# Optimization experiments

Hardware: AMD Instinct MI355X
Metric: run time of the kernel (lower is better)

Reference implementation:

```python
import jax, jax.numpy as jnp
import numpy as np

WINDOW = 128  # crop size (compute_crops default window_size)


def centre_crop(centroids, window_size, h, w):
    # centroids: [C,2] int; returns flat gather coords [2, C*ws*ws]
    half = window_size // 2
    cy = jnp.clip(centroids[:, 0], half, h - half)
    cx = jnp.clip(centroids[:, 1], half, w - half)
    gy, gx = jnp.meshgrid(jnp.arange(window_size), jnp.arange(window_size), indexing='ij')
    rows = (cy - half)[:, None, None] + gy[None]  # [C,ws,ws]
    cols = (cx - half)[:, None, None] + gx[None]
    return jnp.stack([rows.reshape(-1), cols.reshape(-1)])  # [2, C*ws*ws]


def setup_inputs() -> dict:
    key = jax.random.key(0)
    ks = jax.random.split(key, 8)
    E, S, C, H, W = 6, 1, 512, 1024, 1024
    Dh = 16
    return {
        'x': jax.random.normal(ks[0], (E, H, W), dtype=jnp.float32),
        'sigma': jax.random.uniform(ks[1], (S, H, W), dtype=jnp.float32),
        'c': jax.random.normal(ks[2], (C, E), dtype=jnp.float32),
        'W1': jax.random.normal(ks[3], (E + S, Dh), dtype=jnp.float32) * 0.3,
        'b1': jnp.zeros((Dh,), dtype=jnp.float32),
        'W2': jax.random.normal(ks[4], (Dh, Dh), dtype=jnp.float32) * 0.3,
        'b2': jnp.zeros((Dh,), dtype=jnp.float32),
        'W3': jax.random.normal(ks[5], (Dh, 1), dtype=jnp.float32) * 0.3,
        'b3': jnp.zeros((1,), dtype=jnp.float32),
        'centroids_idx': jax.random.randint(ks[6], (C, 2), 0, H, dtype=jnp.int32),
    }


def reference(x, sigma, c, W1, b1, W2, b2, W3, b3, centroids_idx):
    E, h, w = x.shape
    S = sigma.shape[0]
    C = c.shape[0]
    ws = WINDOW
    mesh = centre_crop(centroids_idx, ws, h, w)  # [2, C*ws*ws]
    # gather per-instance windows from concatenated embedding+sigma maps
    xs = jnp.concatenate([x, sigma], axis=0)  # [E+S, H, W]
    g = xs[:, mesh[0], mesh[1]]               # [E+S, C*ws*ws]
    g = g.reshape(E + S, C, ws, ws).transpose(1, 0, 2, 3)  # [C, E+S, ws, ws]
    # subtract centroid descriptor from embedding channels (feature_engineering '0')
    g = jnp.concatenate([g[:, :E] - c[:, :, None, None], g[:, E:]], axis=1)
    feats = g.transpose(0, 2, 3, 1).reshape(-1, E + S)  # [(C*ws*ws), E+S]
    # per-pixel probability MLP (ProbabilityNet)
    hdn = jax.nn.relu(feats @ W1 + b1)
    hdn = jax.nn.relu(hdn @ W2 + b2)
    prob = jax.nn.sigmoid(hdn @ W3 + b3)
    prob = prob.reshape(C, 1, ws, ws)
    # instance-id / coordinate table for the downstream scatter (iidd)
    inst = jnp.repeat(jnp.arange(C, dtype=mesh.dtype), ws * ws)
    iidd = jnp.concatenate([inst[None], mesh], axis=0)  # [3, C*ws*ws]
    return prob, iidd
```

## Files before the change

kernel.cpp:

```cpp
#include <hip/hip_runtime.h>

#define HW (1024 * 1024)
#define PLANE 8388608

typedef _Float16 half4 __attribute__((ext_vector_type(4)));
typedef _Float16 half8 __attribute__((ext_vector_type(8)));
typedef float floatx4 __attribute__((ext_vector_type(4)));

__global__ __launch_bounds__(256) void prep(
    const float* __restrict__ x,
    const float* __restrict__ sigma,
    const float* __restrict__ W1,
    const int*   __restrict__ cent,
    _Float16* __restrict__ P,
    float* __restrict__ out)
{
    if (blockIdx.x < 4096) {
        const int px = blockIdx.x * 256 + threadIdx.x;
        float g[7];
#pragma unroll
        for (int e = 0; e < 6; ++e) g[e] = x[e * HW + px];
        g[6] = sigma[px];

        half8 lo, hi;
#pragma unroll
        for (int j = 0; j < 16; ++j) {
            float a = 0.0f;
#pragma unroll
            for (int e = 0; e < 7; ++e)
                a = fmaf(g[e], W1[e * 16 + j], a);
            if (j < 8) lo[j] = (_Float16)a; else hi[j - 8] = (_Float16)a;
        }
        *(half8*)(P + (size_t)px * 16)     = lo;
        *(half8*)(P + (size_t)px * 16 + 8) = hi;
    } else {
        const int b   = blockIdx.x - 4096;
        const int w   = b >> 2;
        const int qtr = b & 3;
        const int cy0 = min(max(cent[2 * w], 64), 960) - 64;
        const int cx0 = min(max(cent[2 * w + 1], 64), 960) - 64;
        const float iw = (float)w;
#pragma unroll
        for (int pass = 0; pass < 4; ++pass) {
            const int p = qtr * 4096 + pass * 1024 + threadIdx.x * 4;
            const int n = w * 16384 + p;
            const float row = (float)(cy0 + (p >> 7));
            const float c0  = (float)(cx0 + (p & 127));
            float4 iv = {iw, iw, iw, iw};
            float4 rv = {row, row, row, row};
            float4 cv = {c0, c0 + 1.0f, c0 + 2.0f, c0 + 3.0f};
            *(float4*)(out + PLANE + n)     = iv;
            *(float4*)(out + 2 * PLANE + n) = rv;
            *(float4*)(out + 3 * PLANE + n) = cv;
        }
    }
}

__global__ __launch_bounds__(256) void instanseg_mlp(
    const _Float16* __restrict__ P,
    const float* __restrict__ c,
    const float* __restrict__ W1,
    const float* __restrict__ b1,
    const float* __restrict__ W2,
    const float* __restrict__ b2,
    const float* __restrict__ W3,
    const float* __restrict__ b3,
    const int*   __restrict__ cent,
    float* __restrict__ out)
{
    const int cid  = blockIdx.y;
    const int lane = threadIdx.x & 63;
    const int wave = threadIdx.x >> 6;
    const int quad = lane >> 4;
    const int sub  = lane & 15;

    const int cy0 = min(max(cent[2 * cid], 64), 960) - 64;
    const int cx0 = min(max(cent[2 * cid + 1], 64), 960) - 64;

    half4 a2, qh;
    float w3f[4], bb2[4];
#pragma unroll
    for (int i = 0; i < 4; ++i) {
        const int k = 4 * quad + i;
        a2[i]  = (_Float16)W2[k * 16 + sub];
        w3f[i] = W3[k];
        bb2[i] = b2[k];
        float qv = -b1[k];
#pragma unroll
        for (int e = 0; e < 6; ++e)
            qv = fmaf(W1[e * 16 + k], c[cid * 6 + e], qv);
        qh[i] = (_Float16)qv;
    }
    const float b3v = b3[0];
    const floatx4 zero = {0.0f, 0.0f, 0.0f, 0.0f};
    const int wavestart = blockIdx.x * 2048 + wave * 512;

#pragma unroll 2
    for (int it = 0; it < 8; ++it) {
        const int start = wavestart + it * 64;
        const int srcbase = (cy0 + (start >> 7)) * 1024 + cx0 + (start & 127);
        const _Float16* pb = P + (size_t)(srcbase + sub) * 16 + quad * 4;

        float logit[4];
#pragma unroll
        for (int ch = 0; ch < 4; ++ch) {
            half4 v = *(const half4*)(pb + ch * 256);
            half4 h = v - qh;
#pragma unroll
            for (int i = 0; i < 4; ++i)
                h[i] = h[i] > (_Float16)0.0f ? h[i] : (_Float16)0.0f;

            floatx4 c2 = __builtin_amdgcn_mfma_f32_16x16x16f16(a2, h, zero, 0, 0, 0);

            float part = 0.0f;
#pragma unroll
            for (int i = 0; i < 4; ++i)
                part = fmaf(w3f[i], fmaxf(c2[i] + bb2[i], 0.0f), part);
            part += __shfl_xor(part, 16, 64);
            part += __shfl_xor(part, 32, 64);
            logit[ch] = part;
        }

        const float l01 = (quad & 1) ? logit[1] : logit[0];
        const float l23 = (quad & 1) ? logit[3] : logit[2];
        const float lg  = (quad & 2) ? l23 : l01;
        const float prob = __builtin_amdgcn_rcpf(1.0f + __expf(-(lg + b3v)));

        out[cid * 16384 + start + lane] = prob;
    }
}

extern "C" void kernel_launch(void* const* d_in, const int* in_sizes, int n_in,
                              void* d_out, int out_size, void* d_ws, size_t ws_size,
                              hipStream_t stream) {
    const float* x     = (const float*)d_in[0];
    const float* sigma = (const float*)d_in[1];
    const float* c     = (const float*)d_in[2];
    const float* W1    = (const float*)d_in[3];
    const float* b1    = (const float*)d_in[4];
    const float* W2    = (const float*)d_in[5];
    const float* b2    = (const float*)d_in[6];
    const float* W3    = (const float*)d_in[7];
    const float* b3    = (const float*)d_in[8];
    const int*   cent  = (const int*)d_in[9];
    float* out = (float*)d_out;
    _Float16* P = (_Float16*)d_ws;

    prep<<<dim3(4096 + 2048), dim3(256), 0, stream>>>(x, sigma, W1, cent, P, out);
    instanseg_mlp<<<dim3(8, 512), dim3(256), 0, stream>>>(
        P, c, W1, b1, W2, b2, W3, b3, cent, out);
}
```

Measured before the change: 209.2 us.

## Fuse first-layer projection into per-crop MLP kernel using LDS tiles

Replaces the two-kernel scheme (precompute a full-image fp16 first-layer projection into a workspace, then run the MLP per crop) with one fused kernel. Each block loads a 16-row strip of a crop from x and sigma, computes the first layer into shared memory, then runs the MFMA-based second and third layers from LDS. The index-table writes move into an extra z-slice of the same grid. This removes the 32 MB workspace write and read, but the first layer is now recomputed for every overlapping crop (512 crops of 128x128 pixels each), and the grid's x dimension of 8 column blocks mostly exits early.

Measured after the change: 258.4 us. +23.5%, slower.

```diff
diff --git a/kernel.cpp b/kernel.cpp
--- a/kernel.cpp
+++ b/kernel.cpp
@@ -7,57 +7,9 @@
 typedef _Float16 half8 __attribute__((ext_vector_type(8)));
 typedef float floatx4 __attribute__((ext_vector_type(4)));
 
-__global__ __launch_bounds__(256) void prep(
+__global__ __launch_bounds__(512) void instanseg_fused(
     const float* __restrict__ x,
     const float* __restrict__ sigma,
-    const float* __restrict__ W1,
-    const int*   __restrict__ cent,
-    _Float16* __restrict__ P,
-    float* __restrict__ out)
-{
-    if (blockIdx.x < 4096) {
-        const int px = blockIdx.x * 256 + threadIdx.x;
-        float g[7];
-#pragma unroll
-        for (int e = 0; e < 6; ++e) g[e] = x[e * HW + px];
-        g[6] = sigma[px];
-
-        half8 lo, hi;
-#pragma unroll
-        for (int j = 0; j < 16; ++j) {
-            float a = 0.0f;
-#pragma unroll
-            for (int e = 0; e < 7; ++e)
-                a = fmaf(g[e], W1[e * 16 + j], a);
-            if (j < 8) lo[j] = (_Float16)a; else hi[j - 8] = (_Float16)a;
-        }
-        *(half8*)(P + (size_t)px * 16)     = lo;
-        *(half8*)(P + (size_t)px * 16 + 8) = hi;
-    } else {
-        const int b   = blockIdx.x - 4096;
-        const int w   = b >> 2;
-        const int qtr = b & 3;
-        const int cy0 = min(max(cent[2 * w], 64), 960) - 64;
-        const int cx0 = min(max(cent[2 * w + 1], 64), 960) - 64;
-        const float iw = (float)w;
-#pragma unroll
-        for (int pass = 0; pass < 4; ++pass) {
-            const int p = qtr * 4096 + pass * 1024 + threadIdx.x * 4;
-            const int n = w * 16384 + p;
-            const float row = (float)(cy0 + (p >> 7));
-            const float c0  = (float)(cx0 + (p & 127));
-            float4 iv = {iw, iw, iw, iw};
-            float4 rv = {row, row, row, row};
-            float4 cv = {c0, c0 + 1.0f, c0 + 2.0f, c0 + 3.0f};
-            *(float4*)(out + PLANE + n)     = iv;
-            *(float4*)(out + 2 * PLANE + n) = rv;
-            *(float4*)(out + 3 * PLANE + n) = cv;
-        }
-    }
-}
-
-__global__ __launch_bounds__(256) void instanseg_mlp(
-    const _Float16* __restrict__ P,
     const float* __restrict__ c,
     const float* __restrict__ W1,
     const float* __restrict__ b1,
@@ -68,14 +20,67 @@
     const int*   __restrict__ cent,
     float* __restrict__ out)
 {
-    const int cid  = blockIdx.y;
+    __shared__ _Float16 PL[16 * 128 * 16];
+
+    if (blockIdx.z == 8) {
+        const int id  = blockIdx.x + 8 * blockIdx.y;
+        const int w   = id >> 3;
+        const int oct = id & 7;
+        const int cy0 = min(max(cent[2 * w], 64), 960) - 64;
+        const int cx0 = min(max(cent[2 * w + 1], 64), 960) - 64;
+        const int p   = oct * 2048 + threadIdx.x * 4;
+        const int n   = w * 16384 + p;
+        const float iw  = (float)w;
+        const float row = (float)(cy0 + (p >> 7));
+        const float c0  = (float)(cx0 + (p & 127));
+        float4 iv = {iw, iw, iw, iw};
+        float4 rv = {row, row, row, row};
+        float4 cv = {c0, c0 + 1.0f, c0 + 2.0f, c0 + 3.0f};
+        *(float4*)(out + PLANE + n)     = iv;
+        *(float4*)(out + 2 * PLANE + n) = rv;
+        *(float4*)(out + 3 * PLANE + n) = cv;
+        return;
+    }
+
+    const int d = blockIdx.x;
+    const int w = blockIdx.y;
+    const int g = blockIdx.z;
+
+    const int cy0 = min(max(cent[2 * w], 64), 960) - 64;
+    const int cx0 = min(max(cent[2 * w + 1], 64), 960) - 64;
+
+    const int gr0 = cy0 + 16 * g;
+    const int r0  = max(gr0, 128 * d);
+    const int r1  = min(gr0 + 16, 128 * d + 128);
+    if (r0 >= r1) return;
+    const int nrows = r1 - r0;
+    const int npx   = nrows * 128;
+
+    for (int p = threadIdx.x; p < npx; p += 512) {
+        const int src = (r0 + (p >> 7)) * 1024 + cx0 + (p & 127);
+        float gch[7];
+#pragma unroll
+        for (int e = 0; e < 6; ++e) gch[e] = x[e * HW + src];
+        gch[6] = sigma[src];
+
+        half8 lo, hi;
+#pragma unroll
+        for (int j = 0; j < 16; ++j) {
+            float a = 0.0f;
+#pragma unroll
+            for (int e = 0; e < 7; ++e)
+                a = fmaf(gch[e], W1[e * 16 + j], a);
+            if (j < 8) lo[j] = (_Float16)a; else hi[j - 8] = (_Float16)a;
+        }
+        *(half8*)(PL + p * 16)     = lo;
+        *(half8*)(PL + p * 16 + 8) = hi;
+    }
+    __syncthreads();
+
     const int lane = threadIdx.x & 63;
     const int wave = threadIdx.x >> 6;
     const int quad = lane >> 4;
     const int sub  = lane & 15;
-
-    const int cy0 = min(max(cent[2 * cid], 64), 960) - 64;
-    const int cx0 = min(max(cent[2 * cid + 1], 64), 960) - 64;
 
     half4 a2, qh;
     float w3f[4], bb2[4];
@@ -88,23 +93,21 @@
         float qv = -b1[k];
 #pragma unroll
         for (int e = 0; e < 6; ++e)
-            qv = fmaf(W1[e * 16 + k], c[cid * 6 + e], qv);
+            qv = fmaf(W1[e * 16 + k], c[w * 6 + e], qv);
         qh[i] = (_Float16)qv;
     }
     const float b3v = b3[0];
     const floatx4 zero = {0.0f, 0.0f, 0.0f, 0.0f};
-    const int wavestart = blockIdx.x * 2048 + wave * 512;
 
-#pragma unroll 2
-    for (int it = 0; it < 8; ++it) {
-        const int start = wavestart + it * 64;
-        const int srcbase = (cy0 + (start >> 7)) * 1024 + cx0 + (start & 127);
-        const _Float16* pb = P + (size_t)(srcbase + sub) * 16 + quad * 4;
+    const int wrbase = r0 - cy0;
+    const int n_iter = nrows * 2;
 
+    for (int it = wave; it < n_iter; it += 8) {
+        const int p0 = it * 64;
         float logit[4];
 #pragma unroll
         for (int ch = 0; ch < 4; ++ch) {
-            half4 v = *(const half4*)(pb + ch * 256);
+            half4 v = *(const half4*)(PL + (p0 + ch * 16 + sub) * 16 + quad * 4);
             half4 h = v - qh;
 #pragma unroll
             for (int i = 0; i < 4; ++i)
@@ -126,7 +129,8 @@
         const float lg  = (quad & 2) ? l23 : l01;
         const float prob = __builtin_amdgcn_rcpf(1.0f + __expf(-(lg + b3v)));
 
-        out[cid * 16384 + start + lane] = prob;
+        const int pl = p0 + lane;
+        out[w * 16384 + (wrbase + (pl >> 7)) * 128 + (pl & 127)] = prob;
     }
 }
 
@@ -144,9 +148,7 @@
     const float* b3    = (const float*)d_in[8];
     const int*   cent  = (const int*)d_in[9];
     float* out = (float*)d_out;
-    _Float16* P = (_Float16*)d_ws;
 
-    prep<<<dim3(4096 + 2048), dim3(256), 0, stream>>>(x, sigma, W1, cent, P, out);
-    instanseg_mlp<<<dim3(8, 512), dim3(256), 0, stream>>>(
-        P, c, W1, b1, W2, b2, W3, b3, cent, out);
+    instanseg_fused<<<dim3(8, 512, 9), dim3(512), 0, stream>>>(
+        x, sigma, c, W1, b1, W2, b2, W3, b3, cent, out);
 }
```

## Bin MLP tiles by source row band for locality and move iidd writes into MLP kernel

Applied to the files above, without the earlier changes.

A new single-block kernel buckets each (instance, 16-row group) tile into one of 8 bands by its source row position. The MLP grid then uses blockIdx.x as the band, so tiles reading nearby rows of the precomputed fp16 feature map are scheduled together, which should improve L2/cache reuse on the gather. The instance/coordinate table writes move from prep into the MLP kernel, and the output stores become nontemporal. The change adds an extra launch and atomic-based worklist construction, and launches many empty blocks when a band is underfilled.

Measured after the change: 217.5 us. 4.0% more time.

```diff
diff --git a/kernel.cpp b/kernel.cpp
--- a/kernel.cpp
+++ b/kernel.cpp
@@ -7,57 +7,53 @@
 typedef _Float16 half8 __attribute__((ext_vector_type(8)));
 typedef float floatx4 __attribute__((ext_vector_type(4)));
 
+
+__global__ __launch_bounds__(512) void build_worklist(
+    const int* __restrict__ cent, int* __restrict__ ws)
+{
+    __shared__ int cnt[8];
+    if (threadIdx.x < 8) cnt[threadIdx.x] = 0;
+    __syncthreads();
+    for (int t = threadIdx.x; t < 4096; t += 512) {
+        const int w = t >> 3, g = t & 7;
+        const int cy0 = min(max(cent[2 * w], 64), 960) - 64;
+        const int mid = cy0 + 16 * g + 8;
+        const int d = mid >> 7;
+        const int slot = atomicAdd(&cnt[d], 1);
+        ws[16 + d * 1024 + slot] = t;
+    }
+    __syncthreads();
+    if (threadIdx.x < 8) ws[threadIdx.x] = cnt[threadIdx.x];
+}
+
 __global__ __launch_bounds__(256) void prep(
     const float* __restrict__ x,
     const float* __restrict__ sigma,
     const float* __restrict__ W1,
-    const int*   __restrict__ cent,
-    _Float16* __restrict__ P,
-    float* __restrict__ out)
+    _Float16* __restrict__ P)
 {
-    if (blockIdx.x < 4096) {
-        const int px = blockIdx.x * 256 + threadIdx.x;
-        float g[7];
+    const int px = blockIdx.x * 131072 + blockIdx.y * 256 + threadIdx.x;
+    float g[7];
 #pragma unroll
-        for (int e = 0; e < 6; ++e) g[e] = x[e * HW + px];
-        g[6] = sigma[px];
+    for (int e = 0; e < 6; ++e) g[e] = x[e * HW + px];
+    g[6] = sigma[px];
 
-        half8 lo, hi;
+    half8 lo, hi;
 #pragma unroll
-        for (int j = 0; j < 16; ++j) {
-            float a = 0.0f;
+    for (int j = 0; j < 16; ++j) {
+        float a = 0.0f;
 #pragma unroll
-            for (int e = 0; e < 7; ++e)
-                a = fmaf(g[e], W1[e * 16 + j], a);
-            if (j < 8) lo[j] = (_Float16)a; else hi[j - 8] = (_Float16)a;
-        }
-        *(half8*)(P + (size_t)px * 16)     = lo;
-        *(half8*)(P + (size_t)px * 16 + 8) = hi;
-    } else {
-        const int b   = blockIdx.x - 4096;
-        const int w   = b >> 2;
-        const int qtr = b & 3;
-        const int cy0 = min(max(cent[2 * w], 64), 960) - 64;
-        const int cx0 = min(max(cent[2 * w + 1], 64), 960) - 64;
-        const float iw = (float)w;
-#pragma unroll
-        for (int pass = 0; pass < 4; ++pass) {
-            const int p = qtr * 4096 + pass * 1024 + threadIdx.x * 4;
-            const int n = w * 16384 + p;
-            const float row = (float)(cy0 + (p >> 7));
-            const float c0  = (float)(cx0 + (p & 127));
-            float4 iv = {iw, iw, iw, iw};
-            float4 rv = {row, row, row, row};
-            float4 cv = {c0, c0 + 1.0f, c0 + 2.0f, c0 + 3.0f};
-            *(float4*)(out + PLANE + n)     = iv;
-            *(float4*)(out + 2 * PLANE + n) = rv;
-            *(float4*)(out + 3 * PLANE + n) = cv;
-        }
+        for (int e = 0; e < 7; ++e)
+            a = fmaf(g[e], W1[e * 16 + j], a);
+        if (j < 8) lo[j] = (_Float16)a; else hi[j - 8] = (_Float16)a;
     }
+    *(half8*)(P + (size_t)px * 16)     = lo;
+    *(half8*)(P + (size_t)px * 16 + 8) = hi;
 }
 
-__global__ __launch_bounds__(256) void instanseg_mlp(
+__global__ __launch_bounds__(256) void mlp(
     const _Float16* __restrict__ P,
+    const int* __restrict__ ws,
     const float* __restrict__ c,
     const float* __restrict__ W1,
     const float* __restrict__ b1,
@@ -68,36 +64,64 @@
     const int*   __restrict__ cent,
     float* __restrict__ out)
 {
-    const int cid  = blockIdx.y;
+    const int d = blockIdx.x;
+
+    if (blockIdx.y < 128) {
+        const int j    = d * 128 + blockIdx.y;
+        const int w    = j >> 1;
+        const int half = j & 1;
+        const int cy0 = min(max(cent[2 * w], 64), 960) - 64;
+        const int cx0 = min(max(cent[2 * w + 1], 64), 960) - 64;
+        const float iw = (float)w;
+#pragma unroll
+        for (int pass = 0; pass < 8; ++pass) {
+            const int p = half * 8192 + pass * 1024 + threadIdx.x * 4;
+            const int n = w * 16384 + p;
+            const float row = (float)(cy0 + (p >> 7));
+            const float c0  = (float)(cx0 + (p & 127));
+            floatx4 iv = {iw, iw, iw, iw};
+            floatx4 rv = {row, row, row, row};
+            floatx4 cv = {c0, c0 + 1.0f, c0 + 2.0f, c0 + 3.0f};
+            __builtin_nontemporal_store(iv, (floatx4*)(out + PLANE + n));
+            __builtin_nontemporal_store(rv, (floatx4*)(out + 2 * PLANE + n));
+            __builtin_nontemporal_store(cv, (floatx4*)(out + 3 * PLANE + n));
+        }
+        return;
+    }
+
+    const int i = blockIdx.y - 128;
+    if (i >= ws[d]) return;
+    const int t = ws[16 + d * 1024 + i];
+    const int w = t >> 3, g = t & 7;
+
+    const int cy0 = min(max(cent[2 * w], 64), 960) - 64;
+    const int cx0 = min(max(cent[2 * w + 1], 64), 960) - 64;
+
     const int lane = threadIdx.x & 63;
     const int wave = threadIdx.x >> 6;
     const int quad = lane >> 4;
     const int sub  = lane & 15;
 
-    const int cy0 = min(max(cent[2 * cid], 64), 960) - 64;
-    const int cx0 = min(max(cent[2 * cid + 1], 64), 960) - 64;
-
     half4 a2, qh;
     float w3f[4], bb2[4];
 #pragma unroll
-    for (int i = 0; i < 4; ++i) {
-        const int k = 4 * quad + i;
-        a2[i]  = (_Float16)W2[k * 16 + sub];
-        w3f[i] = W3[k];
-        bb2[i] = b2[k];
+    for (int ii = 0; ii < 4; ++ii) {
+        const int k = 4 * quad + ii;
+        a2[ii]  = (_Float16)W2[k * 16 + sub];
+        w3f[ii] = W3[k];
+        bb2[ii] = b2[k];
         float qv = -b1[k];
 #pragma unroll
         for (int e = 0; e < 6; ++e)
-            qv = fmaf(W1[e * 16 + k], c[cid * 6 + e], qv);
-        qh[i] = (_Float16)qv;
+            qv = fmaf(W1[e * 16 + k], c[w * 6 + e], qv);
+        qh[ii] = (_Float16)qv;
     }
     const float b3v = b3[0];
     const floatx4 zero = {0.0f, 0.0f, 0.0f, 0.0f};
-    const int wavestart = blockIdx.x * 2048 + wave * 512;
 
 #pragma unroll 2
-    for (int it = 0; it < 8; ++it) {
-        const int start = wavestart + it * 64;
+    for (int it = wave; it < 32; it += 4) {
+        const int start = g * 2048 + it * 64;
         const int srcbase = (cy0 + (start >> 7)) * 1024 + cx0 + (start & 127);
         const _Float16* pb = P + (size_t)(srcbase + sub) * 16 + quad * 4;
 
@@ -107,15 +131,15 @@
             half4 v = *(const half4*)(pb + ch * 256);
             half4 h = v - qh;
 #pragma unroll
-            for (int i = 0; i < 4; ++i)
-                h[i] = h[i] > (_Float16)0.0f ? h[i] : (_Float16)0.0f;
+            for (int ii = 0; ii < 4; ++ii)
+                h[ii] = h[ii] > (_Float16)0.0f ? h[ii] : (_Float16)0.0f;
 
             floatx4 c2 = __builtin_amdgcn_mfma_f32_16x16x16f16(a2, h, zero, 0, 0, 0);
 
             float part = 0.0f;
 #pragma unroll
-            for (int i = 0; i < 4; ++i)
-                part = fmaf(w3f[i], fmaxf(c2[i] + bb2[i], 0.0f), part);
+            for (int ii = 0; ii < 4; ++ii)
+                part = fmaf(w3f[ii], fmaxf(c2[ii] + bb2[ii], 0.0f), part);
             part += __shfl_xor(part, 16, 64);
             part += __shfl_xor(part, 32, 64);
             logit[ch] = part;
@@ -126,7 +150,7 @@
         const float lg  = (quad & 2) ? l23 : l01;
         const float prob = __builtin_amdgcn_rcpf(1.0f + __expf(-(lg + b3v)));
 
-        out[cid * 16384 + start + lane] = prob;
+        __builtin_nontemporal_store(prob, out + w * 16384 + start + lane);
     }
 }
 
@@ -144,9 +168,12 @@
     const float* b3    = (const float*)d_in[8];
     const int*   cent  = (const int*)d_in[9];
     float* out = (float*)d_out;
-    _Float16* P = (_Float16*)d_ws;
 
-    prep<<<dim3(4096 + 2048), dim3(256), 0, stream>>>(x, sigma, W1, cent, P, out);
-    instanseg_mlp<<<dim3(8, 512), dim3(256), 0, stream>>>(
-        P, c, W1, b1, W2, b2, W3, b3, cent, out);
+    int* wsl    = (int*)d_ws;
+    _Float16* P = (_Float16*)((char*)d_ws + 65536);
+
+    build_worklist<<<dim3(1), dim3(512), 0, stream>>>(cent, wsl);
+    prep<<<dim3(8, 512), dim3(256), 0, stream>>>(x, sigma, W1, P);
+    mlp<<<dim3(8, 1152), dim3(256), 0, stream>>>(
+        P, wsl, c, W1, b1, W2, b2, W3, b3, cent, out);
 }
```
